# Kernel optimization log

Measured on AMD Instinct MI355X. Metric: run time of the kernel, lower is better.

The kernel has to match this reference:

```python
import jax, jax.numpy as jnp
import numpy as np

B = 8
NUM_HEADS = 32
HEAD_DIM = 128
EMBED = NUM_HEADS * HEAD_DIM  # 4096
MAX_LEN = 4096
CUR_LEN = 4095  # cache position to write the new token
W_SCALE = 0.02


def setup_inputs() -> dict:
    key = jax.random.key(0)
    ks = jax.random.split(key, 8)
    return {
        "x": jax.random.normal(ks[0], (B, EMBED), jnp.float32),
        "k_cache": jax.random.normal(ks[1], (B, NUM_HEADS, MAX_LEN, HEAD_DIM), jnp.float32),
        "v_cache": jax.random.normal(ks[2], (B, NUM_HEADS, MAX_LEN, HEAD_DIM), jnp.float32),
        "Wq": jax.random.normal(ks[3], (EMBED, EMBED), jnp.float32) * W_SCALE,
        "bq": jnp.zeros((EMBED,), jnp.float32),
        "Wk": jax.random.normal(ks[4], (EMBED, EMBED), jnp.float32) * W_SCALE,
        "bk": jnp.zeros((EMBED,), jnp.float32),
        "Wv": jax.random.normal(ks[5], (EMBED, EMBED), jnp.float32) * W_SCALE,
        "bv": jnp.zeros((EMBED,), jnp.float32),
        "Wo": jax.random.normal(ks[6], (EMBED, EMBED), jnp.float32) * W_SCALE,
        "bo": jnp.zeros((EMBED,), jnp.float32),
        "cur_len": CUR_LEN,
    }


def reference(x, k_cache, v_cache, Wq, bq, Wk, bk, Wv, bv, Wo, bo, cur_len):
    bsz = x.shape[0]
    # QKV projections for the single new token; (B, H, 1, D)
    q = (x @ Wq.T + bq).reshape(bsz, NUM_HEADS, 1, HEAD_DIM)
    k = (x @ Wk.T + bk).reshape(bsz, NUM_HEADS, 1, HEAD_DIM)
    v = (x @ Wv.T + bv).reshape(bsz, NUM_HEADS, 1, HEAD_DIM)
    # KVCache.update: write new k/v at cur_len, then attend over first cur_len+1
    k_cache = k_cache.at[:, :, cur_len:cur_len + 1, :].set(k)
    v_cache = v_cache.at[:, :, cur_len:cur_len + 1, :].set(v)
    full_k = k_cache[:, :, :cur_len + 1, :]  # (B, H, S, D)
    full_v = v_cache[:, :, :cur_len + 1, :]
    scale = 1.0 / jnp.sqrt(jnp.float32(HEAD_DIM))
    scores = jnp.einsum('bhqd,bhkd->bhqk', q, full_k) * scale  # (B, H, 1, S)
    probs = jax.nn.softmax(scores, axis=-1)
    attn = jnp.einsum('bhqk,bhkd->bhqd', probs, full_v)  # (B, H, 1, D)
    attn = attn.reshape(bsz, EMBED)
    return attn @ Wo.T + bo
```

## Files before the change

kernel.cpp:

```cpp
#include <hip/hip_runtime.h>

#define EMBED 4096
#define NHEADS 32
#define HDIM 128
#define MAXLEN 4096
#define BATCH 8
#define NSPLIT 16

template<int RPW>
__device__ __forceinline__ void gemm8_body(const float* __restrict__ X,
                                           const float* __restrict__ W,
                                           const float* __restrict__ bias,
                                           float* __restrict__ out, int n)
{
    const int lane = threadIdx.x & 63;

    float acc[RPW][8];
    #pragma unroll
    for (int j = 0; j < RPW; ++j)
        #pragma unroll
        for (int m = 0; m < 8; ++m) acc[j][m] = 0.f;

    const float* wb = W + (size_t)n * EMBED;

    #pragma unroll 1
    for (int i = 0; i < 16; ++i) {
        int c = i * 256 + lane * 4;
        float4 wv[RPW];
        #pragma unroll
        for (int j = 0; j < RPW; ++j)
            wv[j] = *(const float4*)(wb + (size_t)j * EMBED + c);
        #pragma unroll
        for (int m = 0; m < 8; ++m) {
            float4 xv = *(const float4*)(X + (size_t)m * EMBED + c);
            #pragma unroll
            for (int j = 0; j < RPW; ++j) {
                acc[j][m] += xv.x * wv[j].x + xv.y * wv[j].y
                           + xv.z * wv[j].z + xv.w * wv[j].w;
            }
        }
    }

    #pragma unroll
    for (int j = 0; j < RPW; ++j)
        #pragma unroll
        for (int m = 0; m < 8; ++m) {
            float v = acc[j][m];
            #pragma unroll
            for (int off = 32; off > 0; off >>= 1) v += __shfl_xor(v, off, 64);
            if (lane == 0) out[(size_t)m * EMBED + n + j] = v + bias[n + j];
        }
}

__global__ __launch_bounds__(256)
void qkv_kernel(const float* __restrict__ x,
                const float* __restrict__ Wq, const float* __restrict__ bq,
                const float* __restrict__ Wk, const float* __restrict__ bk,
                const float* __restrict__ Wv, const float* __restrict__ bv,
                float* __restrict__ qkv )
{
    const int wave = threadIdx.x >> 6;
    int ng = blockIdx.x * 16 + wave * 4;
    int proj = ng >> 12;
    int n = ng & 4095;
    const float* W = proj == 0 ? Wq : (proj == 1 ? Wk : Wv);
    const float* b = proj == 0 ? bq : (proj == 1 ? bk : bv);
    float* out = qkv + (size_t)proj * (BATCH * EMBED);
    gemm8_body<4>(x, W, b, out, n);
}

__global__ __launch_bounds__(256)
void out_kernel(const float* __restrict__ attn,
                const float* __restrict__ Wo, const float* __restrict__ bo,
                float* __restrict__ out)
{
    const int wave = threadIdx.x >> 6;
    int n = blockIdx.x * 8 + wave * 2;
    gemm8_body<2>(attn, Wo, bo, out, n);
}

__global__ __launch_bounds__(256)
void attn_partial(const float* __restrict__ qkv,
                  const float* __restrict__ kc, const float* __restrict__ vc,
                  const int* __restrict__ clp,
                  float* __restrict__ part_acc,
                  float* __restrict__ part_ms)
{
    __shared__ float accs[8][HDIM];
    __shared__ float mls[8][2];

    const int cl = *clp;
    const int T  = cl + 1;
    const int CH = (T + NSPLIT - 1) / NSPLIT;

    const int bh = blockIdx.x & 255;
    const int sp = blockIdx.x >> 8;
    const int b  = bh >> 5;
    const int h  = bh & 31;
    const int tid = threadIdx.x, w = tid >> 6, lane = tid & 63;
    const int half = lane >> 5, col4 = lane & 31;
    const int g = w * 2 + half;

    const int tstart = sp * CH;
    const int tend   = min(T, tstart + CH);

    const float* q    = qkv + (size_t)b * EMBED + h * HDIM;
    const float* knew = qkv + (size_t)BATCH * EMBED     + (size_t)b * EMBED + h * HDIM;
    const float* vnew = qkv + (size_t)2 * BATCH * EMBED + (size_t)b * EMBED + h * HDIM;
    const float* K = kc + (size_t)bh * MAXLEN * HDIM;
    const float* V = vc + (size_t)bh * MAXLEN * HDIM;

    const float scale = 0.08838834764831845f;
    float4 qv = *(const float4*)(q + col4 * 4);
    qv.x *= scale; qv.y *= scale; qv.z *= scale; qv.w *= scale;

    float m = -3.0e38f, l = 0.f;
    float4 acc = make_float4(0.f, 0.f, 0.f, 0.f);

    for (int base = tstart + g; base < tend; base += 32) {
        float4 kv[4], vv[4];
        #pragma unroll
        for (int u = 0; u < 4; ++u) {
            int t = base + u * 8;
            if (t < tend) {
                const float* kp = (t == cl) ? knew : (K + (size_t)t * HDIM);
                const float* vp = (t == cl) ? vnew : (V + (size_t)t * HDIM);
                kv[u] = *(const float4*)(kp + col4 * 4);
                vv[u] = *(const float4*)(vp + col4 * 4);
            }
        }
        #pragma unroll
        for (int u = 0; u < 4; ++u) {
            int t = base + u * 8;
            if (t < tend) {
                float s = qv.x * kv[u].x + qv.y * kv[u].y
                        + qv.z * kv[u].z + qv.w * kv[u].w;
                #pragma unroll
                for (int off = 16; off > 0; off >>= 1) s += __shfl_xor(s, off, 64);
                float mn   = fmaxf(m, s);
                float corr = __expf(m - mn);
                float p    = __expf(s - mn);
                l = l * corr + p;
                acc.x = acc.x * corr + p * vv[u].x;
                acc.y = acc.y * corr + p * vv[u].y;
                acc.z = acc.z * corr + p * vv[u].z;
                acc.w = acc.w * corr + p * vv[u].w;
                m = mn;
            }
        }
    }

    if (col4 == 0) { mls[g][0] = m; mls[g][1] = l; }
    *(float4*)(&accs[g][col4 * 4]) = acc;
    __syncthreads();

    const size_t pidx = (size_t)bh * NSPLIT + sp;
    if (tid < HDIM) {
        float M = mls[0][0];
        #pragma unroll
        for (int i = 1; i < 8; ++i) M = fmaxf(M, mls[i][0]);
        float L = 0.f, o = 0.f;
        #pragma unroll
        for (int i = 0; i < 8; ++i) {
            float wgt = __expf(mls[i][0] - M);
            L += mls[i][1] * wgt;
            o += accs[i][tid] * wgt;
        }
        part_acc[pidx * HDIM + tid] = o;
        if (tid == 0) {
            part_ms[pidx * 2]     = M;
            part_ms[pidx * 2 + 1] = L;
        }
    }
}

__global__ __launch_bounds__(128)
void combine_kernel(const float* __restrict__ part_acc,
                    const float* __restrict__ part_ms,
                    float* __restrict__ attn)
{
    const int bh = blockIdx.x;
    const int d  = threadIdx.x;

    float m[NSPLIT], s[NSPLIT];
    float gmax = -3.0e38f;
    #pragma unroll
    for (int sp = 0; sp < NSPLIT; ++sp) {
        m[sp] = part_ms[((size_t)bh * NSPLIT + sp) * 2];
        s[sp] = part_ms[((size_t)bh * NSPLIT + sp) * 2 + 1];
        gmax  = fmaxf(gmax, m[sp]);
    }
    float total = 0.f, o = 0.f;
    #pragma unroll
    for (int sp = 0; sp < NSPLIT; ++sp) {
        float wgt = __expf(m[sp] - gmax);
        total += s[sp] * wgt;
        o += part_acc[((size_t)bh * NSPLIT + sp) * HDIM + d] * wgt;
    }
    attn[(size_t)bh * HDIM + d] = o / total;
}

extern "C" void kernel_launch(void* const* d_in, const int* in_sizes, int n_in,
                              void* d_out, int out_size, void* d_ws, size_t ws_size,
                              hipStream_t stream) {
    const float* x  = (const float*)d_in[0];
    const float* kc = (const float*)d_in[1];
    const float* vc = (const float*)d_in[2];
    const float* Wq = (const float*)d_in[3];
    const float* bq = (const float*)d_in[4];
    const float* Wk = (const float*)d_in[5];
    const float* bk = (const float*)d_in[6];
    const float* Wv = (const float*)d_in[7];
    const float* bv = (const float*)d_in[8];
    const float* Wo = (const float*)d_in[9];
    const float* bo = (const float*)d_in[10];
    const int* clp  = (const int*)d_in[11];

    float* out      = (float*)d_out;
    float* qkv      = (float*)d_ws;
    float* attn     = qkv + (size_t)3 * BATCH * EMBED;
    float* part_acc = attn + (size_t)BATCH * EMBED;
    float* part_ms  = part_acc + (size_t)256 * NSPLIT * HDIM;

    hipLaunchKernelGGL(qkv_kernel, dim3(768), dim3(256), 0, stream,
                       x, Wq, bq, Wk, bk, Wv, bv, qkv);
    hipLaunchKernelGGL(attn_partial, dim3(256 * NSPLIT), dim3(256), 0, stream,
                       qkv, kc, vc, clp, part_acc, part_ms);
    hipLaunchKernelGGL(combine_kernel, dim3(256), dim3(128), 0, stream,
                       part_acc, part_ms, attn);
    hipLaunchKernelGGL(out_kernel, dim3(512), dim3(256), 0, stream,
                       attn, Wo, bo, out);
}
```

Before: 269.3 us.

## Double-buffer KV loads and batch online-softmax updates in split attention

Restructures the attention partial loop into a fast path with register double-buffering of K/V rows and a combined softmax update over four tokens per step, which cuts the rescale/exp count and the serial dependency chain. Partial or new-token chunks fall back to a masked path that uses the same step. It also adds nontemporal loads and unroll 2 for the weight GEMMs, and an occupancy hint on the attention kernel. The cost is more register pressure and more code complexity.

```diff
diff --git a/kernel.cpp b/kernel.cpp
--- a/kernel.cpp
+++ b/kernel.cpp
@@ -7,6 +7,8 @@
 #define BATCH 8
 #define NSPLIT 16
 
+typedef float __attribute__((ext_vector_type(4))) f32x4;
+
 template<int RPW>
 __device__ __forceinline__ void gemm8_body(const float* __restrict__ X,
                                            const float* __restrict__ W,
@@ -23,16 +25,16 @@
 
     const float* wb = W + (size_t)n * EMBED;
 
-    #pragma unroll 1
+    #pragma unroll 2
     for (int i = 0; i < 16; ++i) {
         int c = i * 256 + lane * 4;
-        float4 wv[RPW];
+        f32x4 wv[RPW];
         #pragma unroll
         for (int j = 0; j < RPW; ++j)
-            wv[j] = *(const float4*)(wb + (size_t)j * EMBED + c);
+            wv[j] = __builtin_nontemporal_load((const f32x4*)(wb + (size_t)j * EMBED + c));
         #pragma unroll
         for (int m = 0; m < 8; ++m) {
-            float4 xv = *(const float4*)(X + (size_t)m * EMBED + c);
+            f32x4 xv = *(const f32x4*)(X + (size_t)m * EMBED + c);
             #pragma unroll
             for (int j = 0; j < RPW; ++j) {
                 acc[j][m] += xv.x * wv[j].x + xv.y * wv[j].y
@@ -79,7 +81,7 @@
     gemm8_body<2>(attn, Wo, bo, out, n);
 }
 
-__global__ __launch_bounds__(256)
+__global__ __launch_bounds__(256, 4)
 void attn_partial(const float* __restrict__ qkv,
                   const float* __restrict__ kc, const float* __restrict__ vc,
                   const int* __restrict__ clp,
@@ -103,55 +105,107 @@
 
     const int tstart = sp * CH;
     const int tend   = min(T, tstart + CH);
+    const int len    = tend - tstart;
 
     const float* q    = qkv + (size_t)b * EMBED + h * HDIM;
     const float* knew = qkv + (size_t)BATCH * EMBED     + (size_t)b * EMBED + h * HDIM;
     const float* vnew = qkv + (size_t)2 * BATCH * EMBED + (size_t)b * EMBED + h * HDIM;
-    const float* K = kc + (size_t)bh * MAXLEN * HDIM;
-    const float* V = vc + (size_t)bh * MAXLEN * HDIM;
+    const float* K = kc + (size_t)bh * MAXLEN * HDIM + col4 * 4;
+    const float* V = vc + (size_t)bh * MAXLEN * HDIM + col4 * 4;
 
     const float scale = 0.08838834764831845f;
-    float4 qv = *(const float4*)(q + col4 * 4);
-    qv.x *= scale; qv.y *= scale; qv.z *= scale; qv.w *= scale;
+    f32x4 qv = *(const f32x4*)(q + col4 * 4);
+    qv *= scale;
 
     float m = -3.0e38f, l = 0.f;
-    float4 acc = make_float4(0.f, 0.f, 0.f, 0.f);
-
-    for (int base = tstart + g; base < tend; base += 32) {
-        float4 kv[4], vv[4];
-        #pragma unroll
-        for (int u = 0; u < 4; ++u) {
-            int t = base + u * 8;
-            if (t < tend) {
-                const float* kp = (t == cl) ? knew : (K + (size_t)t * HDIM);
-                const float* vp = (t == cl) ? vnew : (V + (size_t)t * HDIM);
-                kv[u] = *(const float4*)(kp + col4 * 4);
-                vv[u] = *(const float4*)(vp + col4 * 4);
-            }
-        }
-        #pragma unroll
-        for (int u = 0; u < 4; ++u) {
-            int t = base + u * 8;
-            if (t < tend) {
-                float s = qv.x * kv[u].x + qv.y * kv[u].y
-                        + qv.z * kv[u].z + qv.w * kv[u].w;
+    f32x4 acc = {0.f, 0.f, 0.f, 0.f};
+
+    auto step = [&](const f32x4* kv, const f32x4* vv, float inv0, float inv1,
+                    float inv2, float inv3) {
+        float s0 = qv.x*kv[0].x + qv.y*kv[0].y + qv.z*kv[0].z + qv.w*kv[0].w;
+        float s1 = qv.x*kv[1].x + qv.y*kv[1].y + qv.z*kv[1].z + qv.w*kv[1].w;
+        float s2 = qv.x*kv[2].x + qv.y*kv[2].y + qv.z*kv[2].z + qv.w*kv[2].w;
+        float s3 = qv.x*kv[3].x + qv.y*kv[3].y + qv.z*kv[3].z + qv.w*kv[3].w;
+        #pragma unroll
+        for (int off = 16; off > 0; off >>= 1) {
+            s0 += __shfl_xor(s0, off, 64);
+            s1 += __shfl_xor(s1, off, 64);
+            s2 += __shfl_xor(s2, off, 64);
+            s3 += __shfl_xor(s3, off, 64);
+        }
+        s0 += inv0; s1 += inv1; s2 += inv2; s3 += inv3;
+        float sb = fmaxf(fmaxf(s0, s1), fmaxf(s2, s3));
+        float mn = fmaxf(m, sb);
+        float corr = __expf(m - mn);
+        float p0 = __expf(s0 - mn), p1 = __expf(s1 - mn);
+        float p2 = __expf(s2 - mn), p3 = __expf(s3 - mn);
+        l = l * corr + ((p0 + p1) + (p2 + p3));
+        float tx = fmaf(p3, vv[3].x, fmaf(p2, vv[2].x, fmaf(p1, vv[1].x, p0 * vv[0].x)));
+        float ty = fmaf(p3, vv[3].y, fmaf(p2, vv[2].y, fmaf(p1, vv[1].y, p0 * vv[0].y)));
+        float tz = fmaf(p3, vv[3].z, fmaf(p2, vv[2].z, fmaf(p1, vv[1].z, p0 * vv[0].z)));
+        float tw = fmaf(p3, vv[3].w, fmaf(p2, vv[2].w, fmaf(p1, vv[1].w, p0 * vv[0].w)));
+        acc.x = fmaf(acc.x, corr, tx);
+        acc.y = fmaf(acc.y, corr, ty);
+        acc.z = fmaf(acc.z, corr, tz);
+        acc.w = fmaf(acc.w, corr, tw);
+        m = mn;
+    };
+
+    const bool fast = (len % 32 == 0) && (cl < tstart || cl >= tend);
+
+    if (fast) {
+        const int nb = len >> 5;
+        if (nb > 0) {
+            const int t0 = tstart + g;
+            f32x4 kA[4], vA[4], kB[4], vB[4];
+            auto ldb = [&](f32x4* kv, f32x4* vv, int tb) {
                 #pragma unroll
-                for (int off = 16; off > 0; off >>= 1) s += __shfl_xor(s, off, 64);
-                float mn   = fmaxf(m, s);
-                float corr = __expf(m - mn);
-                float p    = __expf(s - mn);
-                l = l * corr + p;
-                acc.x = acc.x * corr + p * vv[u].x;
-                acc.y = acc.y * corr + p * vv[u].y;
-                acc.z = acc.z * corr + p * vv[u].z;
-                acc.w = acc.w * corr + p * vv[u].w;
-                m = mn;
-            }
+                for (int u = 0; u < 4; ++u) {
+                    kv[u] = *(const f32x4*)(K + (size_t)(tb + u * 8) * HDIM);
+                    vv[u] = *(const f32x4*)(V + (size_t)(tb + u * 8) * HDIM);
+                }
+            };
+            ldb(kA, vA, t0);
+            int j = 0;
+            for (; j + 2 < nb; j += 2) {
+                ldb(kB, vB, t0 + (j + 1) * 32);
+                step(kA, vA, 0.f, 0.f, 0.f, 0.f);
+                ldb(kA, vA, t0 + (j + 2) * 32);
+                step(kB, vB, 0.f, 0.f, 0.f, 0.f);
+            }
+            if (j + 1 < nb) {
+                ldb(kB, vB, t0 + (j + 1) * 32);
+                step(kA, vA, 0.f, 0.f, 0.f, 0.f);
+                step(kB, vB, 0.f, 0.f, 0.f, 0.f);
+            } else {
+                step(kA, vA, 0.f, 0.f, 0.f, 0.f);
+            }
+        }
+    } else {
+        for (int base = tstart + g; base < tend; base += 32) {
+            f32x4 kv[4], vv[4];
+            float inv[4];
+            #pragma unroll
+            for (int u = 0; u < 4; ++u) {
+                int t = base + u * 8;
+                if (t < tend) {
+                    const float* kp = (t == cl) ? (knew + col4 * 4) : (K + (size_t)t * HDIM);
+                    const float* vp = (t == cl) ? (vnew + col4 * 4) : (V + (size_t)t * HDIM);
+                    kv[u] = *(const f32x4*)kp;
+                    vv[u] = *(const f32x4*)vp;
+                    inv[u] = 0.f;
+                } else {
+                    kv[u] = f32x4{0.f, 0.f, 0.f, 0.f};
+                    vv[u] = f32x4{0.f, 0.f, 0.f, 0.f};
+                    inv[u] = -3.0e38f;
+                }
+            }
+            step(kv, vv, inv[0], inv[1], inv[2], inv[3]);
         }
     }
 
     if (col4 == 0) { mls[g][0] = m; mls[g][1] = l; }
-    *(float4*)(&accs[g][col4 * 4]) = acc;
+    *(f32x4*)(&accs[g][col4 * 4]) = acc;
     __syncthreads();
 
     const size_t pidx = (size_t)bh * NSPLIT + sp;
```

After: 277.2 us. 2.9% more time.
